# Kernel tuning notes

Hardware: AMD Instinct MI355X
Metric: run time of the kernel (lower is better)

Reference implementation:

```python
import jax, jax.numpy as jnp
import numpy as np
import itertools

NUM_FRAMES = 8
D = 1024            # img_feature_dim
NB = 256            # num_bottleneck
NC = 400            # num_classes
B = 4096
SCALES = list(range(NUM_FRAMES, 1, -1))  # [8,7,6,5,4,3,2]
SUB = 3


def _relation_indices():
    # Deterministic stand-in for the module's np.random.choice subsampling.
    rng = np.random.default_rng(0)
    sel = []
    for i, scale in enumerate(SCALES):
        rels = list(itertools.combinations(range(NUM_FRAMES), scale))
        if i == 0:
            sel.append(np.array([rels[0]], dtype=np.int32))  # only first relation used
        else:
            n = min(SUB, len(rels))
            idx = rng.choice(len(rels), n, replace=False)
            sel.append(np.array([rels[j] for j in idx], dtype=np.int32))
    return sel

REL = _relation_indices()  # list of [n_sub, scale] int arrays


def setup_inputs() -> dict:
    key = jax.random.key(0)
    ks = jax.random.split(key, 64)
    inp = {"x": jax.random.normal(ks[0], (B, NUM_FRAMES, D), dtype=jnp.float32)}
    k = 1
    for i, scale in enumerate(SCALES):
        inp[f"w1_{i}"] = jax.random.normal(ks[k], (scale * D, NB), dtype=jnp.float32) * 0.02; k += 1
        inp[f"b1_{i}"] = jnp.zeros((NB,), dtype=jnp.float32)
        inp[f"w2_{i}"] = jax.random.normal(ks[k], (NB, NB), dtype=jnp.float32) * 0.02; k += 1
        inp[f"b2_{i}"] = jnp.zeros((NB,), dtype=jnp.float32)
    inp["wc"] = jax.random.normal(ks[k], (NB, NC), dtype=jnp.float32) * 0.02
    inp["bc"] = jnp.zeros((NC,), dtype=jnp.float32)
    return inp


def _fuse(x, rel, w1, b1, w2, b2):
    # x: [B,T,D], rel: [n,scale] frame indices
    n, scale = rel.shape
    g = x[:, rel, :]                              # [B, n, scale, D] gather
    g = g.reshape(x.shape[0], n, scale * D)       # flatten relation features
    h = jax.nn.relu(g)                            # leading ReLU in Sequential
    h = jax.nn.relu(jnp.einsum('bnf,fk->bnk', h, w1) + b1)
    h = jax.nn.relu(jnp.einsum('bnk,kj->bnj', h, w2) + b2)
    # Dropout(p=0.6) is identity in eval mode.
    return h.sum(axis=1)                          # accumulate over subsampled relations


def reference(x,
              w1_0, b1_0, w2_0, b2_0,
              w1_1, b1_1, w2_1, b2_1,
              w1_2, b1_2, w2_2, b2_2,
              w1_3, b1_3, w2_3, b2_3,
              w1_4, b1_4, w2_4, b2_4,
              w1_5, b1_5, w2_5, b2_5,
              w1_6, b1_6, w2_6, b2_6,
              wc, bc):
    w1s = [w1_0, w1_1, w1_2, w1_3, w1_4, w1_5, w1_6]
    b1s = [b1_0, b1_1, b1_2, b1_3, b1_4, b1_5, b1_6]
    w2s = [w2_0, w2_1, w2_2, w2_3, w2_4, w2_5, w2_6]
    b2s = [b2_0, b2_1, b2_2, b2_3, b2_4, b2_5, b2_6]
    act_all = _fuse(x, REL[0], w1s[0], b1s[0], w2s[0], b2s[0])
    for i in range(1, len(SCALES)):
        act_all = act_all + _fuse(x, REL[i], w1s[i], b1s[i], w2s[i], b2s[i])
    out = jax.nn.relu(act_all @ wc + bc)          # classifier: Linear + ReLU
    return out
```

## Files before the change

kernel.cpp:

```cpp
#include <hip/hip_runtime.h>
#include <cstdint>
#include <cstdio>
#include <cstring>

namespace nprng {

struct Pcg64 {
  __uint128_t state, inc;
  bool has_uint32;
  uint32_t uinteger;
  static __uint128_t mult() {
    return (((__uint128_t)0x2360ed051fc65da4ULL) << 64) | 0x4385df649fccf645ULL;
  }
  void step() { state = state * mult() + inc; }
  uint64_t next64() {
    step();
    uint64_t hi = (uint64_t)(state >> 64), lo = (uint64_t)state;
    uint32_t rot = (uint32_t)(state >> 122);
    uint64_t x = hi ^ lo;
    return (x >> rot) | (x << ((64u - rot) & 63u));
  }
  uint32_t next32() {
    if (has_uint32) { has_uint32 = false; return uinteger; }
    uint64_t v = next64();
    has_uint32 = true;
    uinteger = (uint32_t)(v >> 32);
    return (uint32_t)v;
  }
};

static void make_default_rng0(Pcg64& g) {
  const uint32_t INIT_A = 0x43b0d7e5u, MULT_A = 0x931e8875u;
  const uint32_t INIT_B = 0x8b51f9ddu, MULT_B = 0x58f38dedu;
  const uint32_t MIX_L = 0xca01f9ddu, MIX_R = 0x4973f715u;
  uint32_t pool[4];
  uint32_t hc = INIT_A;
  auto hashmix = [&](uint32_t v) -> uint32_t {
    v ^= hc; hc *= MULT_A; v *= hc; v ^= v >> 16; return v;
  };
  auto mix = [&](uint32_t x, uint32_t y) -> uint32_t {
    uint32_t r = x * MIX_L - y * MIX_R; r ^= r >> 16; return r;
  };
  for (int i = 0; i < 4; ++i) pool[i] = hashmix(0u);
  for (int s = 0; s < 4; ++s)
    for (int d = 0; d < 4; ++d)
      if (s != d) pool[d] = mix(pool[d], hashmix(pool[s]));
  uint32_t hb = INIT_B;
  uint32_t w[8];
  for (int i = 0; i < 8; ++i) {
    uint32_t dv = pool[i & 3];
    dv ^= hb; hb *= MULT_B; dv *= hb; dv ^= dv >> 16;
    w[i] = dv;
  }
  uint64_t v64[4];
  for (int i = 0; i < 4; ++i) v64[i] = (uint64_t)w[2 * i] | ((uint64_t)w[2 * i + 1] << 32);
  __uint128_t initstate = (((__uint128_t)v64[0]) << 64) | v64[1];
  __uint128_t initseq   = (((__uint128_t)v64[2]) << 64) | v64[3];
  g.inc = (initseq << 1) | 1;
  g.state = 0; g.has_uint32 = false; g.uinteger = 0;
  g.step();
  g.state += initstate;
  g.step();
}

static uint32_t lemire32(Pcg64& g, uint32_t rng) {
  if (rng == 0) return 0;
  const uint32_t rng_excl = rng + 1u;
  uint64_t m = (uint64_t)g.next32() * (uint64_t)rng_excl;
  uint32_t leftover = (uint32_t)m;
  if (leftover < rng_excl) {
    const uint32_t threshold = (0xFFFFFFFFu - rng) % rng_excl;
    while (leftover < threshold) {
      m = (uint64_t)g.next32() * (uint64_t)rng_excl;
      leftover = (uint32_t)m;
    }
  }
  return (uint32_t)(m >> 32);
}

static void choice3(Pcg64& g, int pop, int64_t out[3]) {
  uint64_t hset[4] = {~0ull, ~0ull, ~0ull, ~0ull};
  const uint64_t mask = 3;
  for (int j = pop - 3; j < pop; ++j) {
    uint64_t val = (uint64_t)lemire32(g, (uint32_t)j);
    uint64_t loc = val & mask;
    while (hset[loc] != ~0ull && hset[loc] != val) loc = (loc + 1) & mask;
    if (hset[loc] == ~0ull) {
      hset[loc] = val;
      out[j - pop + 3] = (int64_t)val;
    } else {
      loc = (uint64_t)j & mask;
      while (hset[loc] != ~0ull) loc = (loc + 1) & mask;
      hset[loc] = (uint64_t)j;
      out[j - pop + 3] = (int64_t)j;
    }
  }
  for (int i = 2; i >= 1; --i) {
    int j = (int)lemire32(g, (uint32_t)i);
    int64_t t = out[i]; out[i] = out[j]; out[j] = t;
  }
}

}

static int all_combos(int s, int combos[80][8]) {
  int c[8];
  for (int i = 0; i < s; ++i) c[i] = i;
  int cnt = 0;
  while (true) {
    for (int i = 0; i < s; ++i) combos[cnt][i] = c[i];
    ++cnt;
    int i = s - 1;
    while (i >= 0 && c[i] == 8 - s + i) --i;
    if (i < 0) break;
    ++c[i];
    for (int j = i + 1; j < s; ++j) c[j] = c[j - 1] + 1;
  }
  return cnt;
}

#define NREL_MAX 19
#define MDIM 4096
#define NB   256
#define NC   400

typedef __attribute__((ext_vector_type(8))) short bf16x8;
typedef __attribute__((ext_vector_type(4))) float f32x4;

__device__ __forceinline__ uint16_t f2bf(float f) {
  uint32_t u = __builtin_bit_cast(uint32_t, f);
  u += 0x7FFFu + ((u >> 16) & 1u);
  return (uint16_t)(u >> 16);
}

__device__ __forceinline__ void gload_lds16(const void* g, void* l) {
  __builtin_amdgcn_global_load_lds(
      (const __attribute__((address_space(1))) unsigned int*)g,
      (__attribute__((address_space(3))) unsigned int*)l, 16, 0, 0);
}


__global__ __launch_bounds__(256) void conv_x_kernel(
    const float* __restrict__ x, uint16_t* __restrict__ xr, int n8)
{
  int i = blockIdx.x * 256 + threadIdx.x;
  const int stride = gridDim.x * 256;
  for (; i < n8; i += stride) {
    const float4 a = ((const float4*)x)[2 * i];
    const float4 b = ((const float4*)x)[2 * i + 1];
    uint32_t p0 = (uint32_t)f2bf(fmaxf(a.x, 0.f)) | ((uint32_t)f2bf(fmaxf(a.y, 0.f)) << 16);
    uint32_t p1 = (uint32_t)f2bf(fmaxf(a.z, 0.f)) | ((uint32_t)f2bf(fmaxf(a.w, 0.f)) << 16);
    uint32_t p2 = (uint32_t)f2bf(fmaxf(b.x, 0.f)) | ((uint32_t)f2bf(fmaxf(b.y, 0.f)) << 16);
    uint32_t p3 = (uint32_t)f2bf(fmaxf(b.z, 0.f)) | ((uint32_t)f2bf(fmaxf(b.w, 0.f)) << 16);
    ((uint4*)xr)[i] = make_uint4(p0, p1, p2, p3);
  }
}

struct ConvTArgs { const float* src[7]; uint16_t* dst[7]; int K[7]; };

__global__ __launch_bounds__(256) void conv_wT_kernel(ConvTArgs a) {
  const int g = blockIdx.z;
  const int K = a.K[g];
  const int k0 = blockIdx.x * 32;
  if (k0 >= K) return;
  const int n0 = blockIdx.y * 32;
  __shared__ float t[32][33];
  const int tr = threadIdx.x >> 5;
  const int tc = threadIdx.x & 31;
  const float* src = a.src[g];
#pragma unroll
  for (int i = 0; i < 4; ++i) {
    const int r = tr + i * 8;
    t[r][tc] = src[(size_t)(k0 + r) * NB + n0 + tc];
  }
  __syncthreads();
  uint16_t* dst = a.dst[g];
#pragma unroll
  for (int i = 0; i < 4; ++i) {
    const int r = tr + i * 8;
    dst[(size_t)(n0 + r) * K + k0 + tc] = f2bf(t[tc][r]);
  }
}

struct G1F {
  const uint16_t* w1T[NREL_MAX];
  const float*    b1[NREL_MAX];
  unsigned char frames[NREL_MAX][8];
  unsigned char scale[NREL_MAX];
};
struct G2F {
  const uint16_t* w2T[NREL_MAX];
  const float*    b2[NREL_MAX];
};

__global__ __launch_bounds__(256) void gemm1_mfma(
    const uint16_t* __restrict__ xr,
    uint16_t* __restrict__ h1,
    G1F args, int zbase)
{
  __shared__ __align__(16) uint16_t sA[128 * 32];
  __shared__ __align__(16) uint16_t sB[128 * 32];
  const int zl  = blockIdx.z;
  const int rel = zbase + zl;
  const int m0  = blockIdx.x * 128;
  const int n0  = blockIdx.y * 128;
  const int scale = (int)args.scale[rel];
  const uint16_t* __restrict__ w1T = args.w1T[rel];
  const int K = scale << 10;

  const int tid  = threadIdx.x;
  const int l    = tid & 63;
  const int w    = tid >> 6;
  const int wm   = w >> 1, wn = w & 1;
  const int lcol = l & 15;
  const int kgrp = (l >> 4) << 3;
  const int srow = tid >> 2;
  const int sko  = (tid & 3) << 3;
  const int ldsoff = (tid >> 6) << 10;

  f32x4 acc[4][4] = {};

  const uint16_t* xbA  = xr + (size_t)(m0 + srow) * 8192 + sko;
  const uint16_t* xbA2 = xr + (size_t)(m0 + 64 + srow) * 8192 + sko;
  const uint16_t* wbB  = w1T + (size_t)(n0 + srow) * K + sko;
  const uint16_t* wbB2 = w1T + (size_t)(n0 + 64 + srow) * K + sko;

  for (int fi = 0; fi < scale; ++fi) {
    const int fr = (int)args.frames[rel][fi];
    const uint16_t* xa  = xbA  + fr * 1024;
    const uint16_t* xa2 = xbA2 + fr * 1024;
    const uint16_t* wb  = wbB  + (fi << 10);
    const uint16_t* wb2 = wbB2 + (fi << 10);
    for (int kc = 0; kc < 1024; kc += 32) {
      gload_lds16(xa  + kc, (char*)sA + ldsoff);
      gload_lds16(xa2 + kc, (char*)sA + 4096 + ldsoff);
      gload_lds16(wb  + kc, (char*)sB + ldsoff);
      gload_lds16(wb2 + kc, (char*)sB + 4096 + ldsoff);
      asm volatile("s_waitcnt vmcnt(0)" ::: "memory");
      __syncthreads();
      bf16x8 af[4], bv[4];
#pragma unroll
      for (int i = 0; i < 4; ++i) {
        af[i] = *(const bf16x8*)((const char*)sA + (((wm << 6) + (i << 4) + lcol) << 6) + (kgrp << 1));
        bv[i] = *(const bf16x8*)((const char*)sB + (((wn << 6) + (i << 4) + lcol) << 6) + (kgrp << 1));
      }
#pragma unroll
      for (int i = 0; i < 4; ++i)
#pragma unroll
        for (int j = 0; j < 4; ++j)
          acc[i][j] = __builtin_amdgcn_mfma_f32_16x16x32_bf16(af[i], bv[j], acc[i][j], 0, 0, 0);
      __syncthreads();
    }
  }

  const float* b1 = args.b1[rel];
  float b1v[4];
#pragma unroll
  for (int j = 0; j < 4; ++j) b1v[j] = b1[n0 + (wn << 6) + (j << 4) + lcol];
  const int orow = (l >> 4) << 2;
#pragma unroll
  for (int i = 0; i < 4; ++i) {
#pragma unroll
    for (int q = 0; q < 4; ++q) {
      const int row = m0 + (wm << 6) + (i << 4) + orow + q;
      uint16_t* hp = h1 + ((size_t)zl * MDIM + row) * NB + n0 + (wn << 6) + lcol;
#pragma unroll
      for (int j = 0; j < 4; ++j)
        hp[j << 4] = f2bf(fmaxf(acc[i][j][q] + b1v[j], 0.f));
    }
  }
}

__global__ __launch_bounds__(256) void gemm2_mfma(
    const uint16_t* __restrict__ h1, float* __restrict__ accb,
    G2F args, int zbase, int zcount, int is_first)
{
  __shared__ __align__(16) uint16_t sA[64 * 32];
  __shared__ __align__(16) uint16_t sB[64 * 32];
  const int m0 = blockIdx.x * 64;
  const int n0 = blockIdx.y * 64;
  const int tid  = threadIdx.x;
  const int l    = tid & 63;
  const int w    = tid >> 6;
  const int wm   = w >> 1, wn = w & 1;
  const int lcol = l & 15;
  const int kgrp = (l >> 4) << 3;
  const int srow = tid >> 2;
  const int sko  = (tid & 3) << 3;
  const int ldsoff = (tid >> 6) << 10;

  float tot[2][2][4] = {};

  for (int zl = 0; zl < zcount; ++zl) {
    const int rel = zbase + zl;
    const uint16_t* __restrict__ w2T = args.w2T[rel];
    const uint16_t* ha = h1 + ((size_t)zl * MDIM + m0 + srow) * NB + sko;
    const uint16_t* wb = w2T + (size_t)(n0 + srow) * NB + sko;
    f32x4 acc[2][2] = {};
    for (int k0 = 0; k0 < NB; k0 += 32) {
      gload_lds16(ha + k0, (char*)sA + ldsoff);
      gload_lds16(wb + k0, (char*)sB + ldsoff);
      asm volatile("s_waitcnt vmcnt(0)" ::: "memory");
      __syncthreads();
      bf16x8 af[2], bv[2];
#pragma unroll
      for (int i = 0; i < 2; ++i) {
        af[i] = *(const bf16x8*)((const char*)sA + (((wm << 5) + (i << 4) + lcol) << 6) + (kgrp << 1));
        bv[i] = *(const bf16x8*)((const char*)sB + (((wn << 5) + (i << 4) + lcol) << 6) + (kgrp << 1));
      }
#pragma unroll
      for (int i = 0; i < 2; ++i)
#pragma unroll
        for (int j = 0; j < 2; ++j)
          acc[i][j] = __builtin_amdgcn_mfma_f32_16x16x32_bf16(af[i], bv[j], acc[i][j], 0, 0, 0);
      __syncthreads();
    }
    const float* b2 = args.b2[rel];
    float b2v[2];
#pragma unroll
    for (int j = 0; j < 2; ++j) b2v[j] = b2[n0 + (wn << 5) + (j << 4) + lcol];
#pragma unroll
    for (int i = 0; i < 2; ++i)
#pragma unroll
      for (int j = 0; j < 2; ++j)
#pragma unroll
        for (int q = 0; q < 4; ++q)
          tot[i][j][q] += fmaxf(acc[i][j][q] + b2v[j], 0.f);
  }

  const int orow = (l >> 4) << 2;
#pragma unroll
  for (int i = 0; i < 2; ++i) {
#pragma unroll
    for (int q = 0; q < 4; ++q) {
      const int row = m0 + (wm << 5) + (i << 4) + orow + q;
      float* ap = accb + (size_t)row * NB + n0 + (wn << 5) + lcol;
#pragma unroll
      for (int j = 0; j < 2; ++j) {
        float v = tot[i][j][q];
        if (!is_first) v += ap[j << 4];
        ap[j << 4] = v;
      }
    }
  }
}

#define MTILE 64
#define NTILE 64
#define KTILE 32
#define LSTR  68

struct G1Args {
  const float* w1[NREL_MAX];
  const float* b1[NREL_MAX];
  unsigned char frames[NREL_MAX][8];
  unsigned char scale[NREL_MAX];
};
struct G2Args {
  const float* w2[NREL_MAX];
  const float* b2[NREL_MAX];
};

__global__ __launch_bounds__(256) void gemm1_kernel(
    const float* __restrict__ x, float* __restrict__ h1, G1Args args, int zbase)
{
  const int zl  = blockIdx.z;
  const int rel = zbase + zl;
  const int m0  = blockIdx.x * MTILE;
  const int n0  = blockIdx.y * NTILE;
  const int K   = ((int)args.scale[rel]) << 10;
  const float* __restrict__ w1 = args.w1[rel];

  __shared__ float As[KTILE][LSTR];
  __shared__ float Bs[KTILE][LSTR];

  const int tid = threadIdx.x;
  const int tx = tid & 15, ty = tid >> 4;
  const int lkA = tid & 31, lmA = tid >> 5;
  const int lnB = tid & 63, lkB = tid >> 6;

  float acc[4][4] = {};

  for (int k0 = 0; k0 < K; k0 += KTILE) {
    const int fr = (int)args.frames[rel][k0 >> 10];
    const float* xp = x + (size_t)m0 * 8192 + (size_t)fr * 1024 + (k0 & 1023) + lkA;
#pragma unroll
    for (int r = 0; r < 8; ++r) {
      float v = xp[(size_t)(lmA + r * 8) * 8192];
      As[lkA][lmA + r * 8] = fmaxf(v, 0.f);
    }
    const float* wp = w1 + (size_t)(k0 + lkB) * NB + n0 + lnB;
#pragma unroll
    for (int r = 0; r < 8; ++r)
      Bs[lkB + r * 4][lnB] = wp[(size_t)r * 4 * NB];
    __syncthreads();
#pragma unroll
    for (int k = 0; k < KTILE; ++k) {
      const float4 av = *(const float4*)&As[k][ty << 2];
      const float4 bvv = *(const float4*)&Bs[k][tx << 2];
      const float ar[4] = {av.x, av.y, av.z, av.w};
      const float br[4] = {bvv.x, bvv.y, bvv.z, bvv.w};
#pragma unroll
      for (int r = 0; r < 4; ++r)
#pragma unroll
        for (int c = 0; c < 4; ++c)
          acc[r][c] = fmaf(ar[r], br[c], acc[r][c]);
    }
    __syncthreads();
  }

  const float* b1p = args.b1[rel] + n0 + (tx << 2);
  const float4 bias = {b1p[0], b1p[1], b1p[2], b1p[3]};
  float* outp = h1 + ((size_t)zl * MDIM + m0 + (ty << 2)) * NB + n0 + (tx << 2);
#pragma unroll
  for (int r = 0; r < 4; ++r) {
    float4 o;
    o.x = fmaxf(acc[r][0] + bias.x, 0.f);
    o.y = fmaxf(acc[r][1] + bias.y, 0.f);
    o.z = fmaxf(acc[r][2] + bias.z, 0.f);
    o.w = fmaxf(acc[r][3] + bias.w, 0.f);
    *(float4*)(outp + (size_t)r * NB) = o;
  }
}

__global__ __launch_bounds__(256) void gemm2_kernel(
    const float* __restrict__ h1, float* __restrict__ accb,
    G2Args args, int zbase, int zcount, int is_first)
{
  const int m0 = blockIdx.x * MTILE;
  const int n0 = blockIdx.y * NTILE;

  __shared__ float As[KTILE][LSTR];
  __shared__ float Bs[KTILE][LSTR];

  const int tid = threadIdx.x;
  const int tx = tid & 15, ty = tid >> 4;
  const int lkA = tid & 31, lmA = tid >> 5;
  const int lnB = tid & 63, lkB = tid >> 6;

  float total[4][4] = {};

  for (int zl = 0; zl < zcount; ++zl) {
    const int rel = zbase + zl;
    const float* __restrict__ w2 = args.w2[rel];
    float acc[4][4] = {};
    for (int k0 = 0; k0 < NB; k0 += KTILE) {
      const float* hp = h1 + ((size_t)zl * MDIM + m0) * NB + k0 + lkA;
#pragma unroll
      for (int r = 0; r < 8; ++r)
        As[lkA][lmA + r * 8] = hp[(size_t)(lmA + r * 8) * NB];
      const float* wp = w2 + (size_t)(k0 + lkB) * NB + n0 + lnB;
#pragma unroll
      for (int r = 0; r < 8; ++r)
        Bs[lkB + r * 4][lnB] = wp[(size_t)r * 4 * NB];
      __syncthreads();
#pragma unroll
      for (int k = 0; k < KTILE; ++k) {
        const float4 av = *(const float4*)&As[k][ty << 2];
        const float4 bvv = *(const float4*)&Bs[k][tx << 2];
        const float ar[4] = {av.x, av.y, av.z, av.w};
        const float br[4] = {bvv.x, bvv.y, bvv.z, bvv.w};
#pragma unroll
        for (int r = 0; r < 4; ++r)
#pragma unroll
          for (int c = 0; c < 4; ++c)
            acc[r][c] = fmaf(ar[r], br[c], acc[r][c]);
      }
      __syncthreads();
    }
    const float* b2p = args.b2[rel] + n0 + (tx << 2);
    const float b2v[4] = {b2p[0], b2p[1], b2p[2], b2p[3]};
#pragma unroll
    for (int r = 0; r < 4; ++r)
#pragma unroll
      for (int c = 0; c < 4; ++c)
        total[r][c] += fmaxf(acc[r][c] + b2v[c], 0.f);
  }

  float* outp = accb + (size_t)(m0 + (ty << 2)) * NB + n0 + (tx << 2);
#pragma unroll
  for (int r = 0; r < 4; ++r) {
    float4 cur;
    if (is_first) { cur.x = cur.y = cur.z = cur.w = 0.f; }
    else          { cur = *(float4*)(outp + (size_t)r * NB); }
    cur.x += total[r][0];
    cur.y += total[r][1];
    cur.z += total[r][2];
    cur.w += total[r][3];
    *(float4*)(outp + (size_t)r * NB) = cur;
  }
}

__global__ __launch_bounds__(256) void gemm3_kernel(
    const float* __restrict__ accb, const float* __restrict__ wc,
    const float* __restrict__ bc, float* __restrict__ out)
{
  const int m0 = blockIdx.x * MTILE;
  const int n0 = blockIdx.y * NTILE;

  __shared__ float As[KTILE][LSTR];
  __shared__ float Bs[KTILE][LSTR];

  const int tid = threadIdx.x;
  const int tx = tid & 15, ty = tid >> 4;
  const int lkA = tid & 31, lmA = tid >> 5;
  const int lnB = tid & 63, lkB = tid >> 6;

  float acc[4][4] = {};

  for (int k0 = 0; k0 < NB; k0 += KTILE) {
    const float* hp = accb + (size_t)m0 * NB + k0 + lkA;
#pragma unroll
    for (int r = 0; r < 8; ++r)
      As[lkA][lmA + r * 8] = hp[(size_t)(lmA + r * 8) * NB];
    const int col = n0 + lnB;
#pragma unroll
    for (int r = 0; r < 8; ++r) {
      float v = 0.f;
      if (col < NC) v = wc[(size_t)(k0 + lkB + r * 4) * NC + col];
      Bs[lkB + r * 4][lnB] = v;
    }
    __syncthreads();
#pragma unroll
    for (int k = 0; k < KTILE; ++k) {
      const float4 av = *(const float4*)&As[k][ty << 2];
      const float4 bvv = *(const float4*)&Bs[k][tx << 2];
      const float ar[4] = {av.x, av.y, av.z, av.w};
      const float br[4] = {bvv.x, bvv.y, bvv.z, bvv.w};
#pragma unroll
      for (int r = 0; r < 4; ++r)
#pragma unroll
        for (int c = 0; c < 4; ++c)
          acc[r][c] = fmaf(ar[r], br[c], acc[r][c]);
    }
    __syncthreads();
  }

#pragma unroll
  for (int r = 0; r < 4; ++r) {
    const int row = m0 + (ty << 2) + r;
#pragma unroll
    for (int c = 0; c < 4; ++c) {
      const int col = n0 + (tx << 2) + c;
      if (col < NC)
        out[(size_t)row * NC + col] = fmaxf(acc[r][c] + bc[col], 0.f);
    }
  }
}

extern "C" void kernel_launch(void* const* d_in, const int* in_sizes, int n_in,
                              void* d_out, int out_size, void* d_ws, size_t ws_size,
                              hipStream_t stream) {
  {
    nprng::Pcg64 chk; nprng::make_default_rng0(chk);
    double r0 = (double)(chk.next64() >> 11) * (1.0 / 9007199254740992.0);
    if (!(r0 > 0.6369616872 && r0 < 0.6369616874))
      fprintf(stderr, "[kernel] WARNING: PCG64 self-check failed: %.17g\n", r0);
  }

  int rel_frames[NREL_MAX][8];
  int rel_scale[NREL_MAX];
  int rel_group[NREL_MAX];
  int n_rel = 0;
  for (int j = 0; j < 8; ++j) rel_frames[0][j] = j;
  rel_scale[0] = 8; rel_group[0] = 0; n_rel = 1;

  nprng::Pcg64 rng; nprng::make_default_rng0(rng);
  for (int gi = 1; gi <= 6; ++gi) {
    const int scale = 8 - gi;
    int combos[80][8];
    const int pop = all_combos(scale, combos);
    int64_t idx[3];
    nprng::choice3(rng, pop, idx);
    for (int t = 0; t < 3; ++t) {
      for (int j = 0; j < 8; ++j) rel_frames[n_rel][j] = (j < scale) ? combos[idx[t]][j] : 0;
      rel_scale[n_rel] = scale;
      rel_group[n_rel] = gi;
      ++n_rel;
    }
  }

  const float* x  = (const float*)d_in[0];
  const float* wc = (const float*)d_in[29];
  const float* bc = (const float*)d_in[30];

  const size_t ACC_B   = (size_t)MDIM * NB * 4;
  const size_t XR_B    = (size_t)MDIM * 8 * 1024 * 2;
  const size_t W1T_B   = (size_t)35 * 1024 * NB * 2;
  const size_t W2T_B   = (size_t)7 * NB * NB * 2;
  const size_t H1REL_B = (size_t)MDIM * NB * 2;
  const size_t off_acc = 0;
  const size_t off_xr  = off_acc + ACC_B;
  const size_t off_w1t = off_xr + XR_B;
  const size_t off_w2t = off_w1t + W1T_B;
  const size_t off_h1  = off_w2t + W2T_B;
  const size_t need_fast = off_h1 + H1REL_B;

  float* accb = (float*)((char*)d_ws + off_acc);

  if (ws_size >= need_fast) {
    uint16_t* xr = (uint16_t*)((char*)d_ws + off_xr);
    uint16_t* h1 = (uint16_t*)((char*)d_ws + off_h1);
    int zcap = (int)((ws_size - off_h1) / H1REL_B);
    if (zcap > n_rel) zcap = n_rel;

    uint16_t* w1t_g[7];
    size_t o = off_w1t;
    for (int g = 0; g < 7; ++g) {
      w1t_g[g] = (uint16_t*)((char*)d_ws + o);
      o += (size_t)(8 - g) * 1024 * NB * 2;
    }
    uint16_t* w2t_g[7];
    for (int g = 0; g < 7; ++g)
      w2t_g[g] = (uint16_t*)((char*)d_ws + off_w2t + (size_t)g * NB * NB * 2);

    conv_x_kernel<<<4096, 256, 0, stream>>>(x, xr, (int)(MDIM * 8 * 1024 / 8));
    ConvTArgs c1, c2;
    for (int g = 0; g < 7; ++g) {
      c1.src[g] = (const float*)d_in[1 + 4 * g];
      c1.dst[g] = w1t_g[g];
      c1.K[g]   = (8 - g) * 1024;
      c2.src[g] = (const float*)d_in[3 + 4 * g];
      c2.dst[g] = w2t_g[g];
      c2.K[g]   = NB;
    }
    conv_wT_kernel<<<dim3(256, 8, 7), 256, 0, stream>>>(c1);
    conv_wT_kernel<<<dim3(8, 8, 7), 256, 0, stream>>>(c2);

    G1F g1; G2F g2;
    memset(&g1, 0, sizeof(g1)); memset(&g2, 0, sizeof(g2));
    for (int r = 0; r < n_rel; ++r) {
      const int gi = rel_group[r];
      g1.w1T[r] = w1t_g[gi];
      g1.b1[r]  = (const float*)d_in[2 + 4 * gi];
      g2.w2T[r] = w2t_g[gi];
      g2.b2[r]  = (const float*)d_in[4 + 4 * gi];
      for (int j = 0; j < 8; ++j) g1.frames[r][j] = (unsigned char)rel_frames[r][j];
      g1.scale[r] = (unsigned char)rel_scale[r];
    }

    int zbase = 0, first = 1;
    while (zbase < n_rel) {
      const int zc = (n_rel - zbase < zcap) ? (n_rel - zbase) : zcap;
      gemm1_mfma<<<dim3(MDIM / 128, NB / 128, zc), 256, 0, stream>>>(xr, h1, g1, zbase);
      gemm2_mfma<<<dim3(MDIM / 64, NB / 64), 256, 0, stream>>>(h1, accb, g2, zbase, zc, first);
      first = 0;
      zbase += zc;
    }
  } else {
    G1Args g1; G2Args g2;
    memset(&g1, 0, sizeof(g1)); memset(&g2, 0, sizeof(g2));
    for (int r = 0; r < n_rel; ++r) {
      const int gi = rel_group[r];
      g1.w1[r] = (const float*)d_in[1 + 4 * gi];
      g1.b1[r] = (const float*)d_in[2 + 4 * gi];
      g2.w2[r] = (const float*)d_in[3 + 4 * gi];
      g2.b2[r] = (const float*)d_in[4 + 4 * gi];
      for (int j = 0; j < 8; ++j) g1.frames[r][j] = (unsigned char)rel_frames[r][j];
      g1.scale[r] = (unsigned char)rel_scale[r];
    }
    const size_t ACC_ELEMS = (size_t)MDIM * NB;
    float* h1f = (float*)d_ws + ACC_ELEMS;
    size_t avail = ws_size / 4;
    int zcap = 1;
    if (avail > ACC_ELEMS) {
      size_t cap = (avail - ACC_ELEMS) / ACC_ELEMS;
      zcap = (int)(cap < (size_t)n_rel ? cap : (size_t)n_rel);
      if (zcap < 1) zcap = 1;
    }
    int zbase = 0, first = 1;
    while (zbase < n_rel) {
      const int zc = (n_rel - zbase < zcap) ? (n_rel - zbase) : zcap;
      gemm1_kernel<<<dim3(MDIM / MTILE, NB / NTILE, zc), 256, 0, stream>>>(x, h1f, g1, zbase);
      gemm2_kernel<<<dim3(MDIM / MTILE, NB / NTILE), 256, 0, stream>>>(h1f, accb, g2, zbase, zc, first);
      first = 0;
      zbase += zc;
    }
  }

  gemm3_kernel<<<dim3(MDIM / MTILE, (NC + NTILE - 1) / NTILE), 256, 0, stream>>>(
      accb, wc, bc, (float*)d_out);
}
```

Before: 587.3 us.

## Pipeline first GEMM with multi-stage LDS ring and split second GEMM across groups

Replaces the first-layer GEMM with a 512-thread kernel. Each block computes a full 256x256 output tile (all NB columns) per relation, using an 8-slot LDS ring filled by direct global-to-LDS loads, an XOR swizzle against bank conflicts, and MFMA bursts run under raised wave priority with fine-grained barriers. The second GEMM is split over four relation groups that write separate partial buffers, which a small reduction kernel then sums, giving more blocks to run in parallel. The aim is to hide load latency and cut the per-step full synchronisation of the old single-buffered loop. The cost is 128KB of LDS per block, which limits occupancy, plus extra workspace and an extra pass over the partial sums.

```diff
diff --git a/kernel.cpp b/kernel.cpp
--- a/kernel.cpp
+++ b/kernel.cpp
@@ -139,7 +139,6 @@
       (__attribute__((address_space(3))) unsigned int*)l, 16, 0, 0);
 }
 
-
 __global__ __launch_bounds__(256) void conv_x_kernel(
     const float* __restrict__ x, uint16_t* __restrict__ xr, int n8)
 {
@@ -193,20 +192,168 @@
   const float*    b2[NREL_MAX];
 };
 
-__global__ __launch_bounds__(256) void gemm1_mfma(
+__global__ __launch_bounds__(512, 2) void gemm1_8p(
     const uint16_t* __restrict__ xr,
     uint16_t* __restrict__ h1,
     G1F args, int zbase)
 {
-  __shared__ __align__(16) uint16_t sA[128 * 32];
-  __shared__ __align__(16) uint16_t sB[128 * 32];
-  const int zl  = blockIdx.z;
+  __shared__ __align__(16) uint16_t lds[65536];
+  const int zl  = blockIdx.y;
   const int rel = zbase + zl;
-  const int m0  = blockIdx.x * 128;
-  const int n0  = blockIdx.y * 128;
+  const int m0  = blockIdx.x << 8;
   const int scale = (int)args.scale[rel];
+  const int NT  = scale << 4;
+  const int K   = scale << 10;
   const uint16_t* __restrict__ w1T = args.w1T[rel];
-  const int K = scale << 10;
+  const float* __restrict__ b1p = args.b1[rel];
+
+  uint64_t fru = 0;
+#pragma unroll
+  for (int j = 0; j < 8; ++j)
+    fru |= ((uint64_t)args.frames[rel][j]) << (8 * j);
+
+  const int tid  = threadIdx.x;
+  const int l    = tid & 63;
+  const int w    = tid >> 6;
+  const int wm   = w >> 2;
+  const int wn   = w & 3;
+  const int lrow = l & 15;
+  const int lk16 = (l >> 4) << 4;
+
+  auto STAGE = [&](int h) {
+    const int kt = h >> 2, kh = (h >> 1) & 1, isB = h & 1;
+    const int reg = (h & 7) << 14;
+    const int fr = (int)((fru >> ((kt >> 4) << 3)) & 255);
+    const int kbaseA = (fr << 10) + ((kt & 15) << 6) + (kh << 5);
+    const int kbaseB = (kt << 6) + (kh << 5);
+#pragma unroll
+    for (int j = 0; j < 2; ++j) {
+      const int s = ((j << 9) + tid) << 4;
+      const int row = s >> 6;
+      const int kb = (s & 63) ^ ((row & 3) << 4);
+      const uint16_t* g;
+      if (!isB) g = xr + (size_t)(m0 + row) * 8192 + kbaseA + (kb >> 1);
+      else      g = w1T + (size_t)row * K + kbaseB + (kb >> 1);
+      gload_lds16(g, (char*)lds + reg + (j << 13) + ((tid >> 6) << 10));
+    }
+  };
+  auto LDA = [&](int reg, int rf) -> bf16x8 {
+    const int row = (wm << 7) + (rf << 4) + lrow;
+    const int kb = lk16 ^ ((row & 3) << 4);
+    return *(const bf16x8*)((const char*)lds + reg + (row << 6) + kb);
+  };
+  auto LDB = [&](int reg, int cq, int cf) -> bf16x8 {
+    const int col = (wn << 6) + (cq << 5) + (cf << 4) + lrow;
+    const int kb = lk16 ^ ((col & 3) << 4);
+    return *(const bf16x8*)((const char*)lds + reg + (col << 6) + kb);
+  };
+
+  f32x4 acc[8][4] = {};
+
+  asm volatile("s_waitcnt vmcnt(0)" ::: "memory");
+  STAGE(0); STAGE(1); STAGE(2); STAGE(3);
+  asm volatile("s_waitcnt vmcnt(4)" ::: "memory");
+  STAGE(4); STAGE(5); STAGE(6);
+  asm volatile("s_waitcnt vmcnt(6)" ::: "memory");
+  asm volatile("s_barrier" ::: "memory");
+
+  const int HTOT = NT << 2;
+  for (int kt = 0; kt < NT; ++kt) {
+    const int h0 = kt << 2;
+    const int regA0 = ((h0 + 0) & 7) << 14;
+    const int regB0 = ((h0 + 1) & 7) << 14;
+    const int regA1 = ((h0 + 2) & 7) << 14;
+    const int regB1 = ((h0 + 3) & 7) << 14;
+    bf16x8 af[8], bv[2];
+
+#pragma unroll
+    for (int rf = 0; rf < 8; ++rf) af[rf] = LDA(regA0, rf);
+    bv[0] = LDB(regB0, 0, 0); bv[1] = LDB(regB0, 0, 1);
+    if (h0 + 7 < HTOT) STAGE(h0 + 7);
+    asm volatile("s_barrier" ::: "memory");
+    __builtin_amdgcn_sched_barrier(0);
+    __builtin_amdgcn_s_setprio(1);
+#pragma unroll
+    for (int rf = 0; rf < 8; ++rf) {
+      acc[rf][0] = __builtin_amdgcn_mfma_f32_16x16x32_bf16(af[rf], bv[0], acc[rf][0], 0, 0, 0);
+      acc[rf][1] = __builtin_amdgcn_mfma_f32_16x16x32_bf16(af[rf], bv[1], acc[rf][1], 0, 0, 0);
+    }
+    __builtin_amdgcn_s_setprio(0);
+    asm volatile("s_barrier" ::: "memory");
+
+    bv[0] = LDB(regB0, 1, 0); bv[1] = LDB(regB0, 1, 1);
+    if (h0 + 8 < HTOT) STAGE(h0 + 8);
+    asm volatile("s_barrier" ::: "memory");
+    __builtin_amdgcn_sched_barrier(0);
+    __builtin_amdgcn_s_setprio(1);
+#pragma unroll
+    for (int rf = 0; rf < 8; ++rf) {
+      acc[rf][2] = __builtin_amdgcn_mfma_f32_16x16x32_bf16(af[rf], bv[0], acc[rf][2], 0, 0, 0);
+      acc[rf][3] = __builtin_amdgcn_mfma_f32_16x16x32_bf16(af[rf], bv[1], acc[rf][3], 0, 0, 0);
+    }
+    __builtin_amdgcn_s_setprio(0);
+    asm volatile("s_barrier" ::: "memory");
+
+#pragma unroll
+    for (int rf = 0; rf < 8; ++rf) af[rf] = LDA(regA1, rf);
+    bv[0] = LDB(regB1, 0, 0); bv[1] = LDB(regB1, 0, 1);
+    if (h0 + 9 < HTOT) STAGE(h0 + 9);
+    asm volatile("s_barrier" ::: "memory");
+    __builtin_amdgcn_sched_barrier(0);
+    __builtin_amdgcn_s_setprio(1);
+#pragma unroll
+    for (int rf = 0; rf < 8; ++rf) {
+      acc[rf][0] = __builtin_amdgcn_mfma_f32_16x16x32_bf16(af[rf], bv[0], acc[rf][0], 0, 0, 0);
+      acc[rf][1] = __builtin_amdgcn_mfma_f32_16x16x32_bf16(af[rf], bv[1], acc[rf][1], 0, 0, 0);
+    }
+    __builtin_amdgcn_s_setprio(0);
+    asm volatile("s_barrier" ::: "memory");
+
+    bv[0] = LDB(regB1, 1, 0); bv[1] = LDB(regB1, 1, 1);
+    if (h0 + 10 < HTOT) STAGE(h0 + 10);
+    asm volatile("s_barrier" ::: "memory");
+    __builtin_amdgcn_sched_barrier(0);
+    __builtin_amdgcn_s_setprio(1);
+#pragma unroll
+    for (int rf = 0; rf < 8; ++rf) {
+      acc[rf][2] = __builtin_amdgcn_mfma_f32_16x16x32_bf16(af[rf], bv[0], acc[rf][2], 0, 0, 0);
+      acc[rf][3] = __builtin_amdgcn_mfma_f32_16x16x32_bf16(af[rf], bv[1], acc[rf][3], 0, 0, 0);
+    }
+    __builtin_amdgcn_s_setprio(0);
+    if (kt == NT - 2)      asm volatile("s_waitcnt vmcnt(0)" ::: "memory");
+    else if (kt < NT - 2)  asm volatile("s_waitcnt vmcnt(6)" ::: "memory");
+    asm volatile("s_barrier" ::: "memory");
+  }
+
+  float b1v[4];
+#pragma unroll
+  for (int c = 0; c < 4; ++c) b1v[c] = b1p[(wn << 6) + (c << 4) + lrow];
+  const int rsub = (l >> 4) << 2;
+#pragma unroll
+  for (int rf = 0; rf < 8; ++rf) {
+#pragma unroll
+    for (int q = 0; q < 4; ++q) {
+      const int row = m0 + (wm << 7) + (rf << 4) + rsub + q;
+      uint16_t* hp = h1 + ((size_t)zl * MDIM + row) * NB + (wn << 6) + lrow;
+#pragma unroll
+      for (int c = 0; c < 4; ++c)
+        hp[c << 4] = f2bf(fmaxf(acc[rf][c][q] + b1v[c], 0.f));
+    }
+  }
+}
+
+__global__ __launch_bounds__(256) void gemm2_mfma(
+    const uint16_t* __restrict__ h1, float* __restrict__ partials,
+    G2F args, int zbase, int zcount, int gsz, int is_first)
+{
+  __shared__ __align__(16) uint16_t sA[64 * 32];
+  __shared__ __align__(16) uint16_t sB[64 * 32];
+  const int m0 = blockIdx.x * 64;
+  const int n0 = blockIdx.y * 64;
+  const int grp = blockIdx.z;
+  const int z0 = grp * gsz;
+  int z1 = z0 + gsz; if (z1 > zcount) z1 = zcount;
+  float* outb = partials + (size_t)grp * MDIM * NB;
 
   const int tid  = threadIdx.x;
   const int l    = tid & 63;
@@ -218,80 +365,9 @@
   const int sko  = (tid & 3) << 3;
   const int ldsoff = (tid >> 6) << 10;
 
-  f32x4 acc[4][4] = {};
-
-  const uint16_t* xbA  = xr + (size_t)(m0 + srow) * 8192 + sko;
-  const uint16_t* xbA2 = xr + (size_t)(m0 + 64 + srow) * 8192 + sko;
-  const uint16_t* wbB  = w1T + (size_t)(n0 + srow) * K + sko;
-  const uint16_t* wbB2 = w1T + (size_t)(n0 + 64 + srow) * K + sko;
-
-  for (int fi = 0; fi < scale; ++fi) {
-    const int fr = (int)args.frames[rel][fi];
-    const uint16_t* xa  = xbA  + fr * 1024;
-    const uint16_t* xa2 = xbA2 + fr * 1024;
-    const uint16_t* wb  = wbB  + (fi << 10);
-    const uint16_t* wb2 = wbB2 + (fi << 10);
-    for (int kc = 0; kc < 1024; kc += 32) {
-      gload_lds16(xa  + kc, (char*)sA + ldsoff);
-      gload_lds16(xa2 + kc, (char*)sA + 4096 + ldsoff);
-      gload_lds16(wb  + kc, (char*)sB + ldsoff);
-      gload_lds16(wb2 + kc, (char*)sB + 4096 + ldsoff);
-      asm volatile("s_waitcnt vmcnt(0)" ::: "memory");
-      __syncthreads();
-      bf16x8 af[4], bv[4];
-#pragma unroll
-      for (int i = 0; i < 4; ++i) {
-        af[i] = *(const bf16x8*)((const char*)sA + (((wm << 6) + (i << 4) + lcol) << 6) + (kgrp << 1));
-        bv[i] = *(const bf16x8*)((const char*)sB + (((wn << 6) + (i << 4) + lcol) << 6) + (kgrp << 1));
-      }
-#pragma unroll
-      for (int i = 0; i < 4; ++i)
-#pragma unroll
-        for (int j = 0; j < 4; ++j)
-          acc[i][j] = __builtin_amdgcn_mfma_f32_16x16x32_bf16(af[i], bv[j], acc[i][j], 0, 0, 0);
-      __syncthreads();
-    }
-  }
-
-  const float* b1 = args.b1[rel];
-  float b1v[4];
-#pragma unroll
-  for (int j = 0; j < 4; ++j) b1v[j] = b1[n0 + (wn << 6) + (j << 4) + lcol];
-  const int orow = (l >> 4) << 2;
-#pragma unroll
-  for (int i = 0; i < 4; ++i) {
-#pragma unroll
-    for (int q = 0; q < 4; ++q) {
-      const int row = m0 + (wm << 6) + (i << 4) + orow + q;
-      uint16_t* hp = h1 + ((size_t)zl * MDIM + row) * NB + n0 + (wn << 6) + lcol;
-#pragma unroll
-      for (int j = 0; j < 4; ++j)
-        hp[j << 4] = f2bf(fmaxf(acc[i][j][q] + b1v[j], 0.f));
-    }
-  }
-}
-
-__global__ __launch_bounds__(256) void gemm2_mfma(
-    const uint16_t* __restrict__ h1, float* __restrict__ accb,
-    G2F args, int zbase, int zcount, int is_first)
-{
-  __shared__ __align__(16) uint16_t sA[64 * 32];
-  __shared__ __align__(16) uint16_t sB[64 * 32];
-  const int m0 = blockIdx.x * 64;
-  const int n0 = blockIdx.y * 64;
-  const int tid  = threadIdx.x;
-  const int l    = tid & 63;
-  const int w    = tid >> 6;
-  const int wm   = w >> 1, wn = w & 1;
-  const int lcol = l & 15;
-  const int kgrp = (l >> 4) << 3;
-  const int srow = tid >> 2;
-  const int sko  = (tid & 3) << 3;
-  const int ldsoff = (tid >> 6) << 10;
-
   float tot[2][2][4] = {};
 
-  for (int zl = 0; zl < zcount; ++zl) {
+  for (int zl = z0; zl < z1; ++zl) {
     const int rel = zbase + zl;
     const uint16_t* __restrict__ w2T = args.w2T[rel];
     const uint16_t* ha = h1 + ((size_t)zl * MDIM + m0 + srow) * NB + sko;
@@ -334,7 +410,7 @@
 #pragma unroll
     for (int q = 0; q < 4; ++q) {
       const int row = m0 + (wm << 5) + (i << 4) + orow + q;
-      float* ap = accb + (size_t)row * NB + n0 + (wn << 5) + lcol;
+      float* ap = outb + (size_t)row * NB + n0 + (wn << 5) + lcol;
 #pragma unroll
       for (int j = 0; j < 2; ++j) {
         float v = tot[i][j][q];
@@ -343,6 +419,21 @@
       }
     }
   }
+}
+
+__global__ __launch_bounds__(256) void reduce4_kernel(
+    const float* __restrict__ p, float* __restrict__ accb)
+{
+  const int i = blockIdx.x * 256 + threadIdx.x;
+  const size_t Q = (size_t)MDIM * NB / 4;
+  const float4* p4 = (const float4*)p;
+  float4 a = p4[i], b = p4[i + Q], c = p4[i + 2 * Q], d = p4[i + 3 * Q];
+  float4 o;
+  o.x = a.x + b.x + c.x + d.x;
+  o.y = a.y + b.y + c.y + d.y;
+  o.z = a.z + b.z + c.z + d.z;
+  o.w = a.w + b.w + c.w + d.w;
+  ((float4*)accb)[i] = o;
 }
 
 #define MTILE 64
@@ -589,16 +680,21 @@
   const size_t W1T_B   = (size_t)35 * 1024 * NB * 2;
   const size_t W2T_B   = (size_t)7 * NB * NB * 2;
   const size_t H1REL_B = (size_t)MDIM * NB * 2;
-  const size_t off_acc = 0;
-  const size_t off_xr  = off_acc + ACC_B;
+  const size_t off_xr  = ACC_B;
   const size_t off_w1t = off_xr + XR_B;
   const size_t off_w2t = off_w1t + W1T_B;
-  const size_t off_h1  = off_w2t + W2T_B;
-  const size_t need_fast = off_h1 + H1REL_B;
-
-  float* accb = (float*)((char*)d_ws + off_acc);
-
-  if (ws_size >= need_fast) {
+  const size_t base    = off_w2t + W2T_B;
+
+  float* accb = (float*)d_ws;
+
+  int ngrp;
+  size_t off_part, off_h1;
+  if (ws_size >= base + 4 * ACC_B + H1REL_B)      { ngrp = 4; off_part = base; off_h1 = base + 4 * ACC_B; }
+  else if (ws_size >= base + H1REL_B)             { ngrp = 1; off_part = 0;    off_h1 = base; }
+  else                                            { ngrp = 0; off_part = 0;    off_h1 = 0; }
+
+  if (ngrp > 0) {
+    float*    parts = (ngrp == 4) ? (float*)((char*)d_ws + off_part) : accb;
     uint16_t* xr = (uint16_t*)((char*)d_ws + off_xr);
     uint16_t* h1 = (uint16_t*)((char*)d_ws + off_h1);
     int zcap = (int)((ws_size - off_h1) / H1REL_B);
@@ -642,11 +738,15 @@
     int zbase = 0, first = 1;
     while (zbase < n_rel) {
       const int zc = (n_rel - zbase < zcap) ? (n_rel - zbase) : zcap;
-      gemm1_mfma<<<dim3(MDIM / 128, NB / 128, zc), 256, 0, stream>>>(xr, h1, g1, zbase);
-      gemm2_mfma<<<dim3(MDIM / 64, NB / 64), 256, 0, stream>>>(h1, accb, g2, zbase, zc, first);
+      gemm1_8p<<<dim3(MDIM / 256, zc), 512, 0, stream>>>(xr, h1, g1, zbase);
+      const int gsz = (zc + ngrp - 1) / ngrp;
+      gemm2_mfma<<<dim3(MDIM / 64, NB / 64, ngrp), 256, 0, stream>>>(
+          h1, parts, g2, zbase, zc, gsz, first);
       first = 0;
       zbase += zc;
     }
+    if (ngrp == 4)
+      reduce4_kernel<<<dim3(MDIM * NB / 4 / 256), 256, 0, stream>>>(parts, accb);
   } else {
     G1Args g1; G2Args g2;
     memset(&g1, 0, sizeof(g1)); memset(&g2, 0, sizeof(g2));
```

Result: no change. 582.2 us (-0.9%).
